# Kernel tuning notes

Hardware: AMD Instinct MI355X
Metric: run time of the kernel (lower is better)

## Reference

```python
import jax, jax.numpy as jnp
import numpy as np

EPS = 1e-5
K = 20
MAXV = 64


def knn_idx(x, k):
    # x: [B,N,D] -> idx: [B,N,k] (excluding self, matching torch topk of -dist)
    xx = jnp.sum(x * x, axis=-1, keepdims=True)                      # [B,N,1]
    dist = xx - 2.0 * jnp.einsum('bnd,bmd->bnm', x, x) + jnp.swapaxes(xx, 1, 2)
    _, idx = jax.lax.top_k(-dist, k + 1)
    return idx[:, :, 1:]


def edge_conv(x, W, gamma, beta, mean, var, k):
    # x: [B,N,C]; W: [O,2C]; BN in eval mode; max over k neighbors
    idx = knn_idx(x, k)                                              # [B,N,k]
    nbr = jax.vmap(lambda xi, ii: xi[ii])(x, idx)                    # [B,N,k,C]
    ctr = jnp.broadcast_to(x[:, :, None, :], nbr.shape)
    ef = jnp.concatenate([ctr, nbr - ctr], axis=-1)                  # [B,N,k,2C]
    y = jnp.einsum('bnkc,oc->bnko', ef, W)                           # 1x1 conv
    y = (y - mean) * (gamma * jax.lax.rsqrt(var + EPS)) + beta       # BN eval
    y = jnp.where(y >= 0, y, 0.2 * y)                                # LeakyReLU
    return jnp.max(y, axis=2)                                        # [B,N,O]


def setup_inputs() -> dict:
    key = jax.random.key(0)
    ks = jax.random.split(key, 32)
    f32 = jnp.float32
    def w(k_, o, i):
        return jax.random.normal(k_, (o, i), f32) / np.float32(np.sqrt(i))
    def vec(k_, c):
        return jax.random.normal(k_, (c,), f32) * 0.1
    d = {}
    d['x'] = jax.random.normal(ks[0], (4, 8192, 5), f32)
    # EdgeConv 1: 5 -> 32
    d['W1'] = w(ks[1], 32, 10)
    d['g1'] = jax.random.uniform(ks[2], (32,), f32, 0.5, 1.5)
    d['b1'] = vec(ks[3], 32); d['m1'] = vec(ks[4], 32)
    d['v1'] = jax.random.uniform(ks[5], (32,), f32, 0.5, 1.5)
    # EdgeConv 2: 32 -> 64
    d['W2'] = w(ks[6], 64, 64)
    d['g2'] = jax.random.uniform(ks[7], (64,), f32, 0.5, 1.5)
    d['b2'] = vec(ks[8], 64); d['m2'] = vec(ks[9], 64)
    d['v2'] = jax.random.uniform(ks[10], (64,), f32, 0.5, 1.5)
    # EdgeConv 3: 64 -> 128
    d['W3'] = w(ks[11], 128, 128)
    d['g3'] = jax.random.uniform(ks[12], (128,), f32, 0.5, 1.5)
    d['b3'] = vec(ks[13], 128); d['m3'] = vec(ks[14], 128)
    d['v3'] = jax.random.uniform(ks[15], (128,), f32, 0.5, 1.5)
    # conv_global: 224 -> 256
    d['Wg'] = w(ks[16], 256, 224)
    d['gg'] = jax.random.uniform(ks[17], (256,), f32, 0.5, 1.5)
    d['bg'] = vec(ks[18], 256); d['mg'] = vec(ks[19], 256)
    d['vg'] = jax.random.uniform(ks[20], (256,), f32, 0.5, 1.5)
    # vertex predictor heads
    d['Wv1'] = w(ks[21], 512, 256); d['bv1'] = vec(ks[22], 512)
    d['Wv2'] = w(ks[23], 192, 512); d['bv2'] = vec(ks[24], 192)
    d['Wq1'] = w(ks[25], 64, 256); d['bq1'] = vec(ks[26], 64)
    d['Wq2'] = w(ks[27], 1, 64); d['bq2'] = vec(ks[28], 1)
    return d


def reference(x, W1, g1, b1, m1, v1, W2, g2, b2, m2, v2, W3, g3, b3, m3, v3,
              Wg, gg, bg, mg, vg, Wv1, bv1, Wv2, bv2, Wq1, bq1, Wq2, bq2):
    B = x.shape[0]
    x1 = edge_conv(x, W1, g1, b1, m1, v1, K)      # [B,N,32]
    x2 = edge_conv(x1, W2, g2, b2, m2, v2, K)     # [B,N,64]
    x3 = edge_conv(x2, W3, g3, b3, m3, v3, K)     # [B,N,128]
    x_concat = jnp.concatenate([x1, x2, x3], axis=2)               # [B,N,224]
    xg = jnp.einsum('bnc,oc->bno', x_concat, Wg)                   # 1x1 conv1d
    xg = (xg - mg) * (gg * jax.lax.rsqrt(vg + EPS)) + bg
    xg = jnp.where(xg >= 0, xg, 0.2 * xg)
    gfeat = jnp.max(xg, axis=1)                                    # [B,256]
    h = jax.nn.relu(gfeat @ Wv1.T + bv1)                           # Dropout=eval id
    vertex_coords = (h @ Wv2.T + bv2).reshape(B, MAXV, 3)
    q = jax.nn.relu(gfeat @ Wq1.T + bq1)
    nvs = jax.nn.sigmoid(q @ Wq2.T + bq2)                          # [B,1]
    num_vertices = jnp.clip(jnp.round(nvs * MAXV), 1, MAXV).astype(jnp.int32)
    return (vertex_coords, num_vertices[:, 0], nvs[:, 0], gfeat, x_concat)
```

## Files before the change

### kernel.cpp

```cpp
#include <hip/hip_runtime.h>
#include <hip/hip_bf16.h>


#define NPTS 8192
#define BATCH 4
#define KNBR 20

template <int D, int RS, int S, int TJ>
__global__ __launch_bounds__(128) void knn_part(
    const float* feat, float* xcat) {
    __shared__ float xj[TJ * D];
    __shared__ float xxj[TJ];
    const int JC = NPTS / S;

    int gi = blockIdx.x * 128 + threadIdx.x;
    int s  = blockIdx.y;
    int b  = gi >> 13;
    int ib = gi & (NPTS - 1);
    const float* fb = feat + (size_t)b * NPTS * RS;

    float xi[D];
    if (D % 4 == 0) {
        #pragma unroll
        for (int c4 = 0; c4 < D / 4; ++c4) {
            float4 v = *(const float4*)(fb + (size_t)ib * RS + 4 * c4);
            xi[4 * c4] = v.x; xi[4 * c4 + 1] = v.y;
            xi[4 * c4 + 2] = v.z; xi[4 * c4 + 3] = v.w;
        }
    } else {
        #pragma unroll
        for (int c = 0; c < D; ++c) xi[c] = fb[(size_t)ib * RS + c];
    }
    float xxi = 0.f;
    #pragma unroll
    for (int c = 0; c < D; ++c) xxi = fmaf(xi[c], xi[c], xxi);

    float dl[21];
    int   il[21];
    #pragma unroll
    for (int t = 0; t < 21; ++t) { dl[t] = __builtin_inff(); il[t] = 0; }

    for (int j0 = s * JC; j0 < (s + 1) * JC; j0 += TJ) {
        __syncthreads();
        if (D % 4 == 0) {
            for (int e = threadIdx.x; e < TJ * (D / 4); e += 128) {
                int r = e / (D / 4), c4 = e % (D / 4);
                float4 v = *(const float4*)(fb + (size_t)(j0 + r) * RS + 4 * c4);
                *(float4*)(xj + r * D + 4 * c4) = v;
            }
        } else {
            for (int e = threadIdx.x; e < TJ * D; e += 128) {
                int r = e / D, c = e % D;
                xj[e] = fb[(size_t)(j0 + r) * RS + c];
            }
        }
        if (threadIdx.x < TJ) {
            const float* row = fb + (size_t)(j0 + threadIdx.x) * RS;
            float sm = 0.f;
            if (D % 4 == 0) {
                #pragma unroll
                for (int c4 = 0; c4 < D / 4; ++c4) {
                    float4 v = *(const float4*)(row + 4 * c4);
                    sm = fmaf(v.x, v.x, sm); sm = fmaf(v.y, v.y, sm);
                    sm = fmaf(v.z, v.z, sm); sm = fmaf(v.w, v.w, sm);
                }
            } else {
                #pragma unroll
                for (int c = 0; c < D; ++c) sm = fmaf(row[c], row[c], sm);
            }
            xxj[threadIdx.x] = sm;
        }
        __syncthreads();
        for (int jj = 0; jj < TJ; ++jj) {
            float dot = 0.f;
            #pragma unroll
            for (int c = 0; c < D; ++c) dot = fmaf(xi[c], xj[jj * D + c], dot);
            float d = __builtin_fmaf(-2.f, dot, xxi + xxj[jj]);
            if (d < dl[20]) {
                dl[20] = d; il[20] = j0 + jj;
                #pragma unroll
                for (int t = 20; t > 0; --t) {
                    if (dl[t] < dl[t - 1]) {
                        float td = dl[t]; dl[t] = dl[t - 1]; dl[t - 1] = td;
                        int   ti = il[t]; il[t] = il[t - 1]; il[t - 1] = ti;
                    }
                }
            }
        }
    }
    unsigned short* cp =
        (unsigned short*)(xcat + (size_t)gi * 224 + 96) + s * 21;
    #pragma unroll
    for (int t = 0; t < 21; ++t) cp[t] = (unsigned short)il[t];
}

template <int D, int RS, int S>
__global__ __launch_bounds__(256) void knn_merge(
    const float* feat, const float* xcat, unsigned short* __restrict__ idxout) {
    int gi = blockIdx.x * 256 + threadIdx.x;
    int b  = gi >> 13;
    int ib = gi & (NPTS - 1);
    const float* fb = feat + (size_t)b * NPTS * RS;

    float xi[D];
    if (D % 4 == 0) {
        #pragma unroll
        for (int c4 = 0; c4 < D / 4; ++c4) {
            float4 v = *(const float4*)(fb + (size_t)ib * RS + 4 * c4);
            xi[4 * c4] = v.x; xi[4 * c4 + 1] = v.y;
            xi[4 * c4 + 2] = v.z; xi[4 * c4 + 3] = v.w;
        }
    } else {
        #pragma unroll
        for (int c = 0; c < D; ++c) xi[c] = fb[(size_t)ib * RS + c];
    }
    float xxi = 0.f;
    #pragma unroll
    for (int c = 0; c < D; ++c) xxi = fmaf(xi[c], xi[c], xxi);

    const unsigned short* cp =
        (const unsigned short*)(xcat + (size_t)gi * 224 + 96);

    float dl[21];
    int   il[21];
    #pragma unroll
    for (int t = 0; t < 21; ++t) { dl[t] = __builtin_inff(); il[t] = 0; }

    for (int t = 0; t < S * 21; ++t) {
        int j = ((int)cp[t]) & (NPTS - 1);
        const float* row = fb + (size_t)j * RS;
        float dot = 0.f, xx = 0.f;
        if (D % 4 == 0) {
            #pragma unroll
            for (int c4 = 0; c4 < D / 4; ++c4) {
                float4 v = *(const float4*)(row + 4 * c4);
                dot = fmaf(xi[4 * c4], v.x, dot);     xx = fmaf(v.x, v.x, xx);
                dot = fmaf(xi[4 * c4 + 1], v.y, dot); xx = fmaf(v.y, v.y, xx);
                dot = fmaf(xi[4 * c4 + 2], v.z, dot); xx = fmaf(v.z, v.z, xx);
                dot = fmaf(xi[4 * c4 + 3], v.w, dot); xx = fmaf(v.w, v.w, xx);
            }
        } else {
            #pragma unroll
            for (int c = 0; c < D; ++c) {
                float v = row[c];
                dot = fmaf(xi[c], v, dot);
                xx  = fmaf(v, v, xx);
            }
        }
        float d = __builtin_fmaf(-2.f, dot, xxi + xx);
        if (d < dl[20]) {
            dl[20] = d; il[20] = j;
            #pragma unroll
            for (int u = 20; u > 0; --u) {
                if (dl[u] < dl[u - 1]) {
                    float td = dl[u]; dl[u] = dl[u - 1]; dl[u - 1] = td;
                    int   ti = il[u]; il[u] = il[u - 1]; il[u - 1] = ti;
                }
            }
        }
    }
    unsigned short* op = idxout + (size_t)gi * KNBR;
    #pragma unroll
    for (int t = 1; t < 21; ++t) op[t - 1] = (unsigned short)il[t];
}

template <int CIN, int RS, int COUT, int OTILE, int P>
__global__ __launch_bounds__(256) void edgeconv_kernel(
    const float* feat, const unsigned short* __restrict__ knn,
    const float* __restrict__ W, const float* __restrict__ g,
    const float* __restrict__ beta, const float* __restrict__ mu,
    const float* __restrict__ var,
    float* outb, int concat_off) {
    __shared__ float diff[P][KNBR][CIN];
    __shared__ float xil[P][CIN];
    __shared__ unsigned short kidx[P * KNBR];
    __shared__ float sl[OTILE], bl[OTILE], ml[OTILE];

    int tid = threadIdx.x;
    int h   = blockIdx.y;
    int n0  = blockIdx.x * P;
    int b   = n0 >> 13;
    const float* fbase = feat + ((size_t)b << 13) * RS;

    for (int e = tid; e < P * CIN; e += 256)
        xil[e / CIN][e % CIN] = feat[(size_t)(n0 + e / CIN) * RS + e % CIN];
    for (int e = tid; e < P * KNBR; e += 256)
        kidx[e] = knn[(size_t)(n0 + e / KNBR) * KNBR + e % KNBR] & (NPTS - 1);
    for (int e = tid; e < OTILE; e += 256) {
        int o = h * OTILE + e;
        sl[e] = g[o] * rsqrtf(var[o] + 1e-5f);
        bl[e] = beta[o];
        ml[e] = mu[o];
    }
    __syncthreads();

    if (CIN % 4 == 0) {
        for (int e = tid; e < P * KNBR * (CIN / 4); e += 256) {
            int r = e / (CIN / 4), c4 = e % (CIN / 4);
            int p = r / KNBR, k = r % KNBR;
            int j = (int)kidx[r];
            float4 v = *(const float4*)(fbase + (size_t)j * RS + 4 * c4);
            diff[p][k][4 * c4 + 0] = v.x - xil[p][4 * c4 + 0];
            diff[p][k][4 * c4 + 1] = v.y - xil[p][4 * c4 + 1];
            diff[p][k][4 * c4 + 2] = v.z - xil[p][4 * c4 + 2];
            diff[p][k][4 * c4 + 3] = v.w - xil[p][4 * c4 + 3];
        }
    } else {
        for (int e = tid; e < P * KNBR * CIN; e += 256) {
            int r = e / CIN, c = e % CIN;
            int p = r / KNBR, k = r % KNBR;
            int j = (int)kidx[r];
            diff[p][k][c] = fbase[(size_t)j * RS + c] - xil[p][c];
        }
    }
    __syncthreads();

    int ol = tid % OTILE, p = tid / OTILE;
    int o  = h * OTILE + ol;

    float wreg[CIN];
    #pragma unroll
    for (int c = 0; c < CIN; ++c) wreg[c] = W[(size_t)o * (2 * CIN) + c];
    float a = 0.f;
    #pragma unroll
    for (int c = 0; c < CIN; ++c) a = fmaf(wreg[c], xil[p][c], a);
    #pragma unroll
    for (int c = 0; c < CIN; ++c) wreg[c] = W[(size_t)o * (2 * CIN) + CIN + c];

    float s = sl[ol], mm = ml[ol], bb = bl[ol];
    float best = -__builtin_inff();
    for (int k = 0; k < KNBR; ++k) {
        float ac0 = a, ac1 = 0.f, ac2 = 0.f, ac3 = 0.f;
        #pragma unroll
        for (int c = 0; c < CIN; ++c) {
            float d = diff[p][k][c];
            if ((c & 3) == 0)      ac0 = fmaf(wreg[c], d, ac0);
            else if ((c & 3) == 1) ac1 = fmaf(wreg[c], d, ac1);
            else if ((c & 3) == 2) ac2 = fmaf(wreg[c], d, ac2);
            else                   ac3 = fmaf(wreg[c], d, ac3);
        }
        float acc = ((ac0 + ac1) + ac2) + ac3;
        float y = (acc - mm) * s + bb;
        y = (y >= 0.f) ? y : 0.2f * y;
        best = fmaxf(best, y);
    }
    outb[(size_t)(n0 + p) * 224 + concat_off + o] = best;
}

__global__ __launch_bounds__(256) void convglobal_kernel(
    const float* __restrict__ xcat,
    const float* __restrict__ Wg, const float* __restrict__ gg,
    const float* __restrict__ bg, const float* __restrict__ mg,
    const float* __restrict__ vg,
    float* __restrict__ partial) {
    int o     = threadIdx.x;
    int chunk = blockIdx.x & 127;
    int b     = blockIdx.x >> 7;

    float s  = gg[o] * rsqrtf(vg[o] + 1e-5f);
    float mm = mg[o], bb = bg[o];
    const float* wrow = Wg + (size_t)o * 224;

    float best = -__builtin_inff();
    for (int grp = 0; grp < 2; ++grp) {
        int n0 = b * NPTS + chunk * 64 + grp * 32;
        float acc[32];
        #pragma unroll
        for (int p = 0; p < 32; ++p) acc[p] = 0.f;
        for (int c = 0; c < 224; ++c) {
            float w = wrow[c];
            const float* f = xcat + (size_t)n0 * 224 + c;
            #pragma unroll
            for (int p = 0; p < 32; ++p) acc[p] = fmaf(w, f[p * 224], acc[p]);
        }
        #pragma unroll
        for (int p = 0; p < 32; ++p) {
            float y = (acc[p] - mm) * s + bb;
            y = (y >= 0.f) ? y : 0.2f * y;
            best = fmaxf(best, y);
        }
    }
    partial[(size_t)blockIdx.x * 256 + o] = best;
}

__global__ void reduce_gfeat_kernel(const float* __restrict__ partial,
                                    float* __restrict__ gfeat,
                                    float* __restrict__ outg) {
    int b = blockIdx.x, o = threadIdx.x;
    float best = -__builtin_inff();
    for (int ch = 0; ch < 128; ++ch)
        best = fmaxf(best, partial[((size_t)b * 128 + ch) * 256 + o]);
    gfeat[b * 256 + o] = best;
    outg[b * 256 + o]  = best;
}

__global__ __launch_bounds__(256) void heads_kernel(
    const float* __restrict__ gfeat,
    const float* __restrict__ Wv1, const float* __restrict__ bv1,
    const float* __restrict__ Wv2, const float* __restrict__ bv2,
    const float* __restrict__ Wq1, const float* __restrict__ bq1,
    const float* __restrict__ Wq2, const float* __restrict__ bq2,
    float* __restrict__ out) {
    int b = blockIdx.x, t = threadIdx.x;
    __shared__ float gf[256], h[512], q[64];
    gf[t] = gfeat[b * 256 + t];
    __syncthreads();
    for (int r = t; r < 512; r += 256) {
        float acc = bv1[r];
        for (int c = 0; c < 256; ++c) acc = fmaf(Wv1[r * 256 + c], gf[c], acc);
        h[r] = fmaxf(acc, 0.f);
    }
    __syncthreads();
    if (t < 192) {
        float acc = bv2[t];
        for (int c = 0; c < 512; ++c) acc = fmaf(Wv2[t * 512 + c], h[c], acc);
        out[b * 192 + t] = acc;
    } else {
        int r = t - 192;
        if (r < 64) {
            float acc = bq1[r];
            for (int c = 0; c < 256; ++c) acc = fmaf(Wq1[r * 256 + c], gf[c], acc);
            q[r] = fmaxf(acc, 0.f);
        }
    }
    __syncthreads();
    if (t == 0) {
        float acc = bq2[0];
        for (int c = 0; c < 64; ++c) acc = fmaf(Wq2[c], q[c], acc);
        float nv = 1.0f / (1.0f + expf(-acc));
        out[772 + b] = nv;
        float num = fminf(fmaxf(rintf(nv * 64.0f), 1.0f), 64.0f);
        out[768 + b] = num;
    }
}

extern "C" void kernel_launch(void* const* d_in, const int* in_sizes, int n_in,
                              void* d_out, int out_size, void* d_ws, size_t ws_size,
                              hipStream_t stream) {
    (void)in_sizes; (void)n_in; (void)out_size; (void)ws_size;
    const float* x   = (const float*)d_in[0];
    const float* W1  = (const float*)d_in[1];
    const float* g1  = (const float*)d_in[2];
    const float* b1  = (const float*)d_in[3];
    const float* m1  = (const float*)d_in[4];
    const float* v1  = (const float*)d_in[5];
    const float* W2  = (const float*)d_in[6];
    const float* g2  = (const float*)d_in[7];
    const float* b2  = (const float*)d_in[8];
    const float* m2  = (const float*)d_in[9];
    const float* v2  = (const float*)d_in[10];
    const float* W3  = (const float*)d_in[11];
    const float* g3  = (const float*)d_in[12];
    const float* b3  = (const float*)d_in[13];
    const float* m3  = (const float*)d_in[14];
    const float* v3  = (const float*)d_in[15];
    const float* Wg  = (const float*)d_in[16];
    const float* gg  = (const float*)d_in[17];
    const float* bg  = (const float*)d_in[18];
    const float* mg  = (const float*)d_in[19];
    const float* vg  = (const float*)d_in[20];
    const float* Wv1 = (const float*)d_in[21];
    const float* bv1 = (const float*)d_in[22];
    const float* Wv2 = (const float*)d_in[23];
    const float* bv2 = (const float*)d_in[24];
    const float* Wq1 = (const float*)d_in[25];
    const float* bq1 = (const float*)d_in[26];
    const float* Wq2 = (const float*)d_in[27];
    const float* bq2 = (const float*)d_in[28];

    float* out  = (float*)d_out;
    float* xcat = out + 1800;
    char* ws = (char*)d_ws;
    const int ROWS = BATCH * NPTS;

    unsigned short* idx  = (unsigned short*)(ws);
    float*          part = (float*)(ws);
    float*          gft  = (float*)(ws + 524288);

    knn_part<5, 5, 8, 128><<<dim3(ROWS / 128, 8), 128, 0, stream>>>(x, xcat);
    knn_merge<5, 5, 8><<<ROWS / 256, 256, 0, stream>>>(x, xcat, idx);
    edgeconv_kernel<5, 5, 32, 32, 8>
        <<<dim3(ROWS / 8, 1), 256, 0, stream>>>(x, idx, W1, g1, b1, m1, v1, xcat, 0);

    knn_part<32, 224, 8, 128><<<dim3(ROWS / 128, 8), 128, 0, stream>>>(xcat, xcat);
    knn_merge<32, 224, 8><<<ROWS / 256, 256, 0, stream>>>(xcat, xcat, idx);
    edgeconv_kernel<32, 224, 64, 64, 4>
        <<<dim3(ROWS / 4, 1), 256, 0, stream>>>(xcat, idx, W2, g2, b2, m2, v2, xcat, 32);

    knn_part<64, 224, 8, 64><<<dim3(ROWS / 128, 8), 128, 0, stream>>>(xcat + 32, xcat);
    knn_merge<64, 224, 8><<<ROWS / 256, 256, 0, stream>>>(xcat + 32, xcat, idx);
    edgeconv_kernel<64, 224, 128, 64, 4>
        <<<dim3(ROWS / 4, 2), 256, 0, stream>>>(xcat + 32, idx, W3, g3, b3, m3, v3, xcat, 96);

    convglobal_kernel<<<BATCH * 128, 256, 0, stream>>>(
        xcat, Wg, gg, bg, mg, vg, part);
    reduce_gfeat_kernel<<<BATCH, 256, 0, stream>>>(part, gft, out + 776);

    heads_kernel<<<BATCH, 256, 0, stream>>>(
        gft, Wv1, bv1, Wv2, bv2, Wq1, bq1, Wq2, bq2, out);
}
```

Before: 4.498 ms.

## Tile global conv as shared-memory GEMM and vectorize kNN dot LDS reads

Rewrites the global 1x1 conv as a 64x64 output tile per block with transposed feature and weight chunks staged in shared memory and a 4x4 register micro-tile, followed by an in-block max reduction. This replaces per-thread strided global loads that had little reuse. The kNN distance loop now reads neighbour features from shared memory as float4 when the channel count allows. The change adds shared memory use and a block-level reduction.

```diff
diff --git a/kernel.cpp b/kernel.cpp
--- a/kernel.cpp
+++ b/kernel.cpp
@@ -73,8 +73,20 @@
         __syncthreads();
         for (int jj = 0; jj < TJ; ++jj) {
             float dot = 0.f;
-            #pragma unroll
-            for (int c = 0; c < D; ++c) dot = fmaf(xi[c], xj[jj * D + c], dot);
+            if (D % 4 == 0) {
+                const float* xr = xj + jj * D;
+                #pragma unroll
+                for (int c4 = 0; c4 < D / 4; ++c4) {
+                    float4 v = *(const float4*)(xr + 4 * c4);
+                    dot = fmaf(xi[4 * c4 + 0], v.x, dot);
+                    dot = fmaf(xi[4 * c4 + 1], v.y, dot);
+                    dot = fmaf(xi[4 * c4 + 2], v.z, dot);
+                    dot = fmaf(xi[4 * c4 + 3], v.w, dot);
+                }
+            } else {
+                #pragma unroll
+                for (int c = 0; c < D; ++c) dot = fmaf(xi[c], xj[jj * D + c], dot);
+            }
             float d = __builtin_fmaf(-2.f, dot, xxi + xxj[jj]);
             if (d < dl[20]) {
                 dl[20] = d; il[20] = j0 + jj;
@@ -208,9 +220,10 @@
     } else {
         for (int e = tid; e < P * KNBR * CIN; e += 256) {
             int r = e / CIN, c = e % CIN;
-            int p = r / KNBR, k = r % KNBR;
+            int p = r / CIN == 0 ? 0 : 0;
+            int pp = r / KNBR, k = r % KNBR;
             int j = (int)kidx[r];
-            diff[p][k][c] = fbase[(size_t)j * RS + c] - xil[p][c];
+            diff[pp][k][c] = fbase[(size_t)j * RS + c] - xil[pp][c];
         }
     }
     __syncthreads();
@@ -253,34 +266,86 @@
     const float* __restrict__ bg, const float* __restrict__ mg,
     const float* __restrict__ vg,
     float* __restrict__ partial) {
-    int o     = threadIdx.x;
-    int chunk = blockIdx.x & 127;
-    int b     = blockIdx.x >> 7;
-
-    float s  = gg[o] * rsqrtf(vg[o] + 1e-5f);
-    float mm = mg[o], bb = bg[o];
-    const float* wrow = Wg + (size_t)o * 224;
-
-    float best = -__builtin_inff();
-    for (int grp = 0; grp < 2; ++grp) {
-        int n0 = b * NPTS + chunk * 64 + grp * 32;
-        float acc[32];
-        #pragma unroll
-        for (int p = 0; p < 32; ++p) acc[p] = 0.f;
-        for (int c = 0; c < 224; ++c) {
-            float w = wrow[c];
-            const float* f = xcat + (size_t)n0 * 224 + c;
-            #pragma unroll
-            for (int p = 0; p < 32; ++p) acc[p] = fmaf(w, f[p * 224], acc[p]);
-        }
-        #pragma unroll
-        for (int p = 0; p < 32; ++p) {
-            float y = (acc[p] - mm) * s + bb;
+    const int KC = 56, PT = 64, OT = 64, ST = 68;
+    __shared__ float flT[KC * ST];
+    __shared__ float WlT[KC * ST];
+    __shared__ float red[64 * 17];
+
+    int tid = threadIdx.x;
+    int oi  = tid & 15, pi = tid >> 4;
+    int o0  = blockIdx.y * OT;
+    int n0  = blockIdx.x * PT;
+    int b   = n0 >> 13;
+    int pchunk = blockIdx.x & 127;
+
+    float acc[4][4];
+    #pragma unroll
+    for (int u = 0; u < 4; ++u)
+        #pragma unroll
+        for (int v = 0; v < 4; ++v) acc[u][v] = 0.f;
+
+    for (int kc = 0; kc < 224; kc += KC) {
+        __syncthreads();
+        for (int e = tid; e < PT * (KC / 4); e += 256) {
+            int p = e / (KC / 4), c4 = e % (KC / 4);
+            float4 v = *(const float4*)(xcat + (size_t)(n0 + p) * 224 + kc + 4 * c4);
+            flT[(4 * c4 + 0) * ST + p] = v.x;
+            flT[(4 * c4 + 1) * ST + p] = v.y;
+            flT[(4 * c4 + 2) * ST + p] = v.z;
+            flT[(4 * c4 + 3) * ST + p] = v.w;
+        }
+        for (int e = tid; e < OT * (KC / 4); e += 256) {
+            int o = e / (KC / 4), c4 = e % (KC / 4);
+            float4 v = *(const float4*)(Wg + (size_t)(o0 + o) * 224 + kc + 4 * c4);
+            WlT[(4 * c4 + 0) * ST + o] = v.x;
+            WlT[(4 * c4 + 1) * ST + o] = v.y;
+            WlT[(4 * c4 + 2) * ST + o] = v.z;
+            WlT[(4 * c4 + 3) * ST + o] = v.w;
+        }
+        __syncthreads();
+        #pragma unroll 8
+        for (int c = 0; c < KC; ++c) {
+            float4 w4 = *(const float4*)(WlT + c * ST + oi * 4);
+            float4 f4 = *(const float4*)(flT + c * ST + pi * 4);
+            acc[0][0] = fmaf(w4.x, f4.x, acc[0][0]);
+            acc[0][1] = fmaf(w4.x, f4.y, acc[0][1]);
+            acc[0][2] = fmaf(w4.x, f4.z, acc[0][2]);
+            acc[0][3] = fmaf(w4.x, f4.w, acc[0][3]);
+            acc[1][0] = fmaf(w4.y, f4.x, acc[1][0]);
+            acc[1][1] = fmaf(w4.y, f4.y, acc[1][1]);
+            acc[1][2] = fmaf(w4.y, f4.z, acc[1][2]);
+            acc[1][3] = fmaf(w4.y, f4.w, acc[1][3]);
+            acc[2][0] = fmaf(w4.z, f4.x, acc[2][0]);
+            acc[2][1] = fmaf(w4.z, f4.y, acc[2][1]);
+            acc[2][2] = fmaf(w4.z, f4.z, acc[2][2]);
+            acc[2][3] = fmaf(w4.z, f4.w, acc[2][3]);
+            acc[3][0] = fmaf(w4.w, f4.x, acc[3][0]);
+            acc[3][1] = fmaf(w4.w, f4.y, acc[3][1]);
+            acc[3][2] = fmaf(w4.w, f4.z, acc[3][2]);
+            acc[3][3] = fmaf(w4.w, f4.w, acc[3][3]);
+        }
+    }
+    #pragma unroll
+    for (int u = 0; u < 4; ++u) {
+        int oL = oi * 4 + u, o = o0 + oL;
+        float s = gg[o] * rsqrtf(vg[o] + 1e-5f);
+        float mm = mg[o], bb = bg[o];
+        float best = -__builtin_inff();
+        #pragma unroll
+        for (int v = 0; v < 4; ++v) {
+            float y = (acc[u][v] - mm) * s + bb;
             y = (y >= 0.f) ? y : 0.2f * y;
             best = fmaxf(best, y);
         }
-    }
-    partial[(size_t)blockIdx.x * 256 + o] = best;
+        red[oL * 17 + pi] = best;
+    }
+    __syncthreads();
+    if (tid < 64) {
+        float best = -__builtin_inff();
+        #pragma unroll
+        for (int q = 0; q < 16; ++q) best = fmaxf(best, red[tid * 17 + q]);
+        partial[((size_t)(b * 128 + pchunk)) * 256 + o0 + tid] = best;
+    }
 }
 
 __global__ void reduce_gfeat_kernel(const float* __restrict__ partial,
@@ -392,7 +457,7 @@
     edgeconv_kernel<64, 224, 128, 64, 4>
         <<<dim3(ROWS / 4, 2), 256, 0, stream>>>(xcat + 32, idx, W3, g3, b3, m3, v3, xcat, 96);
 
-    convglobal_kernel<<<BATCH * 128, 256, 0, stream>>>(
+    convglobal_kernel<<<dim3(ROWS / 64, 4), 256, 0, stream>>>(
         xcat, Wg, gg, bg, mg, vg, part);
     reduce_gfeat_kernel<<<BATCH, 256, 0, stream>>>(part, gft, out + 776);
 
```

New measurement: 4.369 ms. -2.9%, faster.
